# Performance work log

Hardware: AMD Instinct MI355X
Metric: run time of the kernel (lower is better)

## Reference

```python
import jax, jax.numpy as jnp
import numpy as np

GROUP_SIZE = 32
NUM_EMBEDDINGS = 130048
EMBEDDING_DIM = 4096


def setup_inputs() -> dict:
    key = jax.random.key(0)
    k_in, k_w, k_s = jax.random.split(key, 3)
    input_ids = jax.random.randint(k_in, (4, 2048), 0, NUM_EMBEDDINGS, dtype=jnp.int64)
    # packed int4 weights: two rows per byte, low nibble = even index
    weight = jax.random.randint(k_w, (NUM_EMBEDDINGS // 2, EMBEDDING_DIM), 0, 256, dtype=jnp.int32).astype(jnp.uint8)
    # per-group, per-feature dequant scales
    weight_scale = (jax.random.normal(k_s, (NUM_EMBEDDINGS // GROUP_SIZE, EMBEDDING_DIM), dtype=jnp.float32) * 0.02)
    return {"input": input_ids, "weight": weight, "weight_scale": weight_scale}


def reference(input, weight, weight_scale):
    # input: [B, S] int token ids
    group_idx = input // GROUP_SIZE          # [B, S] -> row in scale table
    embed_idx = input // 2                   # [B, S] -> row in packed table
    scales = weight_scale[group_idx]         # [B, S, D]
    packed = weight[embed_idx]               # [B, S, D] uint8
    shifts = ((input % 2) * 4).astype(jnp.uint8)[..., None]  # 0 for even ids (low nibble), 4 for odd
    nibbles = (packed >> shifts) & jnp.uint8(15)             # [B, S, D] in [0, 15]
    deq = (nibbles.astype(jnp.int8) - 8).astype(scales.dtype)  # signed int4 -> [-8, 7]
    return deq * scales                       # [B, S, D] float32
```

## Files before the change

kernel.cpp:

```cpp
#include <hip/hip_runtime.h>

#define EMB_DIM 4096

__global__ __launch_bounds__(256) void qembed_kernel(
    const int* __restrict__ ids,
    const int* __restrict__ weight,
    const float* __restrict__ scale,
    float* __restrict__ out,
    int n_tokens)
{
    const int token = blockIdx.x;
    if (token >= n_tokens) return;

    const int id = ids[token];
    const long long wrow = (long long)(id >> 1) * EMB_DIM;
    const long long srow = (long long)(id >> 5) * EMB_DIM;
    const int shift = (id & 1) * 4;
    const long long obase = (long long)token * EMB_DIM;

    const int f0 = threadIdx.x * 4;

    int4   w[4];
    float4 s[4];
    #pragma unroll
    for (int it = 0; it < 4; ++it) {
        const int f = f0 + it * 1024;
        const int* wp = &weight[wrow + f];
        w[it].x = __builtin_nontemporal_load(&wp[0]);
        w[it].y = __builtin_nontemporal_load(&wp[1]);
        w[it].z = __builtin_nontemporal_load(&wp[2]);
        w[it].w = __builtin_nontemporal_load(&wp[3]);
        s[it] = *reinterpret_cast<const float4*>(&scale[srow + f]);
    }

    #pragma unroll
    for (int it = 0; it < 4; ++it) {
        const int f = f0 + it * 1024;
        float4 o;
        o.x = (float)(((w[it].x >> shift) & 15) - 8) * s[it].x;
        o.y = (float)(((w[it].y >> shift) & 15) - 8) * s[it].y;
        o.z = (float)(((w[it].z >> shift) & 15) - 8) * s[it].z;
        o.w = (float)(((w[it].w >> shift) & 15) - 8) * s[it].w;
        float* op = &out[obase + f];
        __builtin_nontemporal_store(o.x, &op[0]);
        __builtin_nontemporal_store(o.y, &op[1]);
        __builtin_nontemporal_store(o.z, &op[2]);
        __builtin_nontemporal_store(o.w, &op[3]);
    }
}

extern "C" void kernel_launch(void* const* d_in, const int* in_sizes, int n_in,
                              void* d_out, int out_size, void* d_ws, size_t ws_size,
                              hipStream_t stream) {
    const int*   ids    = (const int*)d_in[0];
    const int*   weight = (const int*)d_in[1];
    const float* scale  = (const float*)d_in[2];
    float*       out    = (float*)d_out;

    const int n_tokens = in_sizes[0];
    qembed_kernel<<<n_tokens, 256, 0, stream>>>(ids, weight, scale, out, n_tokens);
}
```

Before: 61.15 us.

## Sort tokens by scale group and remap blocks to improve cache reuse

Adds a single-block counting sort that orders tokens by their scale-group row (id>>5) and packs id and token index into one int. The embedding kernel reads this permutation and also remaps block indices so that adjacent sorted tokens land on the same XCD, so duplicate weight and scale rows can hit in L2. Weight loads switch from nontemporal to normal cached int4 loads. The cost is an extra serial single-block launch and a bit-packing scheme that assumes fewer than 8192 tokens and ids that fit in the remaining bits.

```diff
diff --git a/kernel.cpp b/kernel.cpp
--- a/kernel.cpp
+++ b/kernel.cpp
@@ -1,21 +1,65 @@
 #include <hip/hip_runtime.h>
 
 #define EMB_DIM 4096
+#define NBIN    4096
+
+__global__ __launch_bounds__(1024) void sort_kernel(
+    const int* __restrict__ ids, int* __restrict__ perm, int n_tokens)
+{
+    __shared__ int hist[NBIN];
+    __shared__ int part[1024];
+    const int t = threadIdx.x;
+
+    for (int i = t; i < NBIN; i += 1024) hist[i] = 0;
+    __syncthreads();
+
+    for (int tok = t; tok < n_tokens; tok += 1024)
+        atomicAdd(&hist[ids[tok] >> 5], 1);
+    __syncthreads();
+
+    const int l0 = hist[t*4+0], l1 = hist[t*4+1], l2 = hist[t*4+2], l3 = hist[t*4+3];
+    const int s = l0 + l1 + l2 + l3;
+    part[t] = s;
+    __syncthreads();
+    for (int off = 1; off < 1024; off <<= 1) {
+        int v = (t >= off) ? part[t - off] : 0;
+        __syncthreads();
+        part[t] += v;
+        __syncthreads();
+    }
+    const int base = part[t] - s;
+    hist[t*4+0] = base;
+    hist[t*4+1] = base + l0;
+    hist[t*4+2] = base + l0 + l1;
+    hist[t*4+3] = base + l0 + l1 + l2;
+    __syncthreads();
+
+    for (int tok = t; tok < n_tokens; tok += 1024) {
+        const int id  = ids[tok];
+        const int pos = atomicAdd(&hist[id >> 5], 1);
+        perm[pos] = (id << 13) | tok;
+    }
+}
 
 __global__ __launch_bounds__(256) void qembed_kernel(
-    const int* __restrict__ ids,
+    const int* __restrict__ perm,
     const int* __restrict__ weight,
     const float* __restrict__ scale,
     float* __restrict__ out,
     int n_tokens)
 {
-    const int token = blockIdx.x;
-    if (token >= n_tokens) return;
+    const int b  = blockIdx.x;
+    const int nb = gridDim.x;
+    const int p = ((nb & 7) == 0) ? ((b & 7) * (nb >> 3) + (b >> 3)) : b;
+    if (p >= n_tokens) return;
 
-    const int id = ids[token];
-    const long long wrow = (long long)(id >> 1) * EMB_DIM;
-    const long long srow = (long long)(id >> 5) * EMB_DIM;
-    const int shift = (id & 1) * 4;
+    const int packed = perm[p];
+    const int token  = packed & 8191;
+    const int id     = packed >> 13;
+
+    const long long wrow  = (long long)(id >> 1) * EMB_DIM;
+    const long long srow  = (long long)(id >> 5) * EMB_DIM;
+    const int shift       = (id & 1) * 4;
     const long long obase = (long long)token * EMB_DIM;
 
     const int f0 = threadIdx.x * 4;
@@ -25,11 +69,7 @@
     #pragma unroll
     for (int it = 0; it < 4; ++it) {
         const int f = f0 + it * 1024;
-        const int* wp = &weight[wrow + f];
-        w[it].x = __builtin_nontemporal_load(&wp[0]);
-        w[it].y = __builtin_nontemporal_load(&wp[1]);
-        w[it].z = __builtin_nontemporal_load(&wp[2]);
-        w[it].w = __builtin_nontemporal_load(&wp[3]);
+        w[it] = *reinterpret_cast<const int4*>(&weight[wrow + f]);
         s[it] = *reinterpret_cast<const float4*>(&scale[srow + f]);
     }
 
@@ -56,7 +96,9 @@
     const int*   weight = (const int*)d_in[1];
     const float* scale  = (const float*)d_in[2];
     float*       out    = (float*)d_out;
+    int*         perm   = (int*)d_ws;
 
     const int n_tokens = in_sizes[0];
-    qembed_kernel<<<n_tokens, 256, 0, stream>>>(ids, weight, scale, out, n_tokens);
+    sort_kernel<<<1, 1024, 0, stream>>>(ids, perm, n_tokens);
+    qembed_kernel<<<n_tokens, 256, 0, stream>>>(perm, weight, scale, out, n_tokens);
 }
```

Result: slower. 62.48 us (+2.2%).
